# Optimization experiments

Measured on AMD Instinct MI355X. Metric: run time of the kernel, lower is better.

## Reference

```python
import jax, jax.numpy as jnp
import numpy as np

H1, H2, H3 = 32, 64, 64
NODEN = 12
NODES_PER_GRAPH = NODEN + 2  # 14
N = 700000                   # 50000 graphs * 14 nodes
E = 4000000


def setup_inputs() -> dict:
    key = jax.random.key(0)
    ks = jax.random.split(key, 8)
    x = jax.random.normal(ks[0], (N, H1), dtype=jnp.float32)
    edges = jax.random.randint(ks[1], (2, E), 0, N, dtype=jnp.int64)
    W1 = jax.random.normal(ks[2], (H1, H2), dtype=jnp.float32) / np.sqrt(H1).astype(np.float32)
    b1 = jnp.zeros((H2,), jnp.float32)
    W2 = jax.random.normal(ks[3], (H2, H3), dtype=jnp.float32) / np.sqrt(H2).astype(np.float32)
    b2 = jnp.zeros((H3,), jnp.float32)
    Wfc = jax.random.normal(ks[4], (H3 * NODES_PER_GRAPH, 1), dtype=jnp.float32) / np.sqrt(H3 * NODES_PER_GRAPH).astype(np.float32)
    bfc = jnp.zeros((1,), jnp.float32)
    return {"x": x, "edges": edges, "W1": W1, "b1": b1, "W2": W2, "b2": b2, "Wfc": Wfc, "bfc": bfc}


def gcn_conv(x, src, dst, W, b, n):
    # PyG GCNConv: h = X W; add self-loops; norm = deg^-1/2[src]*deg^-1/2[dst]
    h = x @ W  # [N, out]
    ones = jnp.ones(src.shape[0], dtype=h.dtype)
    deg = jax.ops.segment_sum(ones, dst, num_segments=n) + jnp.asarray(1.0, h.dtype)  # +1 self-loop
    dinv = jax.lax.rsqrt(deg)  # deg >= 1 always (self-loop)
    norm = dinv[src] * dinv[dst]  # [E]
    agg = jax.ops.segment_sum(h[src] * norm[:, None], dst, num_segments=n)
    agg = agg + h * (dinv * dinv)[:, None]  # self-loop contribution
    return agg + b


def reference(x, edges, W1, b1, W2, b2, Wfc, bfc):
    src, dst = edges[0], edges[1]
    h = jax.nn.relu(gcn_conv(x, src, dst, W1, b1, N))
    # F.dropout(training=False) is identity in eval mode
    h = jax.nn.relu(gcn_conv(h, src, dst, W2, b2, N))
    h = h.reshape(-1, H3 * NODES_PER_GRAPH)  # [B, 896]
    return h @ Wfc + bfc  # [B, 1]
```

## Files before the change

### kernel.cpp

```cpp
#include <hip/hip_runtime.h>
#include <hip/hip_fp16.h>


typedef _Float16 half8 __attribute__((ext_vector_type(8)));
typedef float float4v __attribute__((ext_vector_type(4)));

#define CHUNK 8192
#define BSH 11
#define BNODES 2048
#define DBINS 64
#define NBKMAX 512

__global__ __launch_bounds__(256) void fallback_kernel(float* __restrict__ out, int n, float v)
{
  int i = blockIdx.x * 256 + threadIdx.x;
  if (i < n) out[i] = v;
}

__device__ inline int edges_shift(const int* __restrict__ edges)
{
  int orv = edges[1] | edges[3] | edges[5] | edges[7] | edges[9] | edges[11] | edges[13] | edges[15];
  return (orv == 0) ? 1 : 0;
}

__device__ inline void scan_bstart(const int* __restrict__ gtot, int NBK, int* __restrict__ bl)
{
  int t = threadIdx.x;
  if (t < 64) {
    int carry = 0;
    int rounds = (NBK + 63) >> 6;
    for (int r = 0; r < rounds; r++) {
      int idx = r * 64 + t;
      int v = (idx < NBK) ? gtot[idx] : 0;
      int incl = v;
#pragma unroll
      for (int off = 1; off < 64; off <<= 1) {
        int x = __shfl_up(incl, off);
        if (t >= off) incl += x;
      }
      if (idx < NBK) bl[idx] = incl - v + carry;
      carry += __shfl(incl, 63);
    }
    if (t == 0) bl[NBK] = carry;
  }
}

__global__ __launch_bounds__(256) void hist2_kernel(
    const int* __restrict__ edges, int E, int N,
    int* __restrict__ cnt, int NBK, int* __restrict__ gtot,
    __half* __restrict__ P, __half* __restrict__ F2)
{
  __shared__ int lh[NBKMAX];
  int t = threadIdx.x;
  int blk = blockIdx.x;
  if (blk == 0) {
    if (t < 8) ((uint2*)(P + (size_t)N * 32))[t] = make_uint2(0, 0);
    else if (t < 24) ((uint2*)(F2 + (size_t)N * 64))[t - 8] = make_uint2(0, 0);
  }
  for (int b = t; b < NBK; b += 256) lh[b] = 0;
  __syncthreads();
  int sh = edges_shift(edges);
  int base = blk * CHUNK;
#pragma unroll
  for (int k = 0; k < CHUNK / 256; k++) {
    int e = base + k * 256 + t;
    if (e < E) {
      int d = edges[(E + e) << sh];
      if ((unsigned)d < (unsigned)N) atomicAdd(&lh[d >> BSH], 1);
    }
  }
  __syncthreads();
  for (int b = t; b < NBK; b += 256)
    cnt[(size_t)blk * NBK + b] = atomicAdd(&gtot[b], lh[b]);
}

__global__ __launch_bounds__(256) void pass3_kernel(
    const int* __restrict__ edges, int E, int N,
    const int* __restrict__ cnt, const int* __restrict__ gtot,
    int* __restrict__ pair, int NBK)
{
  __shared__ int bl[NBKMAX + 1];
  __shared__ int lcur[NBKMAX];
  int t = threadIdx.x;
  int blk = blockIdx.x;
  scan_bstart(gtot, NBK, bl);
  __syncthreads();
  for (int b = t; b < NBK; b += 256)
    lcur[b] = bl[b] + cnt[(size_t)blk * NBK + b];
  __syncthreads();
  int sh = edges_shift(edges);
  int base = blk * CHUNK;
#pragma unroll
  for (int k = 0; k < CHUNK / 256; k++) {
    int e = base + k * 256 + t;
    if (e < E) {
      int s = edges[e << sh];
      int d = edges[(E + e) << sh];
      if ((unsigned)s < (unsigned)N && (unsigned)d < (unsigned)N) {
        int pos = atomicAdd(&lcur[d >> BSH], 1);
        pair[pos] = s | ((d & (BNODES - 1)) << 20);
      }
    }
  }
}

__global__ __launch_bounds__(256) void build_kernel(
    const int* __restrict__ pair, const int* __restrict__ gtot,
    int* __restrict__ rowptr, float* __restrict__ dinv, int* __restrict__ col,
    int* __restrict__ dhist, int N, int NBK)
{
  __shared__ int bl[NBKMAX + 1];
  __shared__ int hist[BNODES];
  __shared__ int cur[BNODES];
  __shared__ int sc[256];
  __shared__ int lh2[DBINS];
  int b = blockIdx.x;
  int t = threadIdx.x;
  scan_bstart(gtot, NBK, bl);
  if (t < DBINS) lh2[t] = 0;
#pragma unroll
  for (int i = 0; i < BNODES / 256; i++) {
    int idx = i * 256 + t;
    int row = (b << BSH) + idx;
    hist[idx] = (row < N) ? 1 : 0;
  }
  __syncthreads();
  int pbeg = bl[b], pend = bl[b + 1];
  int colbase = pbeg + (b << BSH);
  if (b == 0 && t == 0) rowptr[N] = bl[NBK] + N;
  for (int p = pbeg + t; p < pend; p += 256)
    atomicAdd(&hist[(pair[p] >> 20) & (BNODES - 1)], 1);
  __syncthreads();
  int hv[8];
  int tsum = 0;
#pragma unroll
  for (int i = 0; i < 8; i++) { hv[i] = hist[t * 8 + i]; tsum += hv[i]; }
  sc[t] = tsum;
  __syncthreads();
  for (int off = 1; off < 256; off <<= 1) {
    int x = 0;
    if (t >= off) x = sc[t - off];
    __syncthreads();
    if (t >= off) sc[t] += x;
    __syncthreads();
  }
  int run = sc[t] - tsum;
#pragma unroll
  for (int i = 0; i < 8; i++) {
    int idx = t * 8 + i;
    int rp = colbase + run;
    int row = (b << BSH) + idx;
    if (row < N) {
      rowptr[row] = rp;
      dinv[row] = rsqrtf((float)hv[i]);
      col[rp] = row;
      cur[idx] = rp + 1;
      int bin = hv[i] < DBINS ? hv[i] : DBINS - 1;
      atomicAdd(&lh2[bin], 1);
    } else {
      cur[idx] = rp;
    }
    run += hv[i];
  }
  __syncthreads();
  if (t < DBINS && lh2[t]) atomicAdd(&dhist[t], lh2[t]);
  for (int p = pbeg + t; p < pend; p += 256) {
    int v = pair[p];
    int pos = atomicAdd(&cur[(v >> 20) & (BNODES - 1)], 1);
    col[pos] = v & 0xFFFFF;
  }
}

__global__ __launch_bounds__(256) void deg_place_kernel(
    const int* __restrict__ rowptr, const float* __restrict__ dinv,
    const int* __restrict__ dhist, int* __restrict__ dcnt,
    int* __restrict__ perm, int* __restrict__ iperm,
    int2* __restrict__ rowinfo, float* __restrict__ dinv_p,
    const float* __restrict__ X, __half* __restrict__ P,
    float* __restrict__ out, const float* __restrict__ bfc, int N, int B)
{
  __shared__ int bb[DBINS];
  __shared__ int lh[DBINS];
  __shared__ int lbase[DBINS];
  int t = threadIdx.x;
  int n = blockIdx.x * 256 + t;
  if (n < B) out[n] = bfc[0];
  if (t < DBINS) {
    lh[t] = 0;
    int v = dhist[t];
    int incl = v;
#pragma unroll
    for (int off = 1; off < DBINS; off <<= 1) {
      int x = __shfl_up(incl, off);
      if (t >= off) incl += x;
    }
    bb[t] = incl - v;
  }
  __syncthreads();
  int b = -1, rbeg = 0, rlen = 0;
  if (n < N) {
    rbeg = rowptr[n];
    rlen = rowptr[n + 1] - rbeg;
    b = rlen < DBINS ? rlen : DBINS - 1;
    atomicAdd(&lh[b], 1);
  }
  __syncthreads();
  if (t < DBINS) lbase[t] = lh[t] ? (bb[t] + atomicAdd(&dcnt[t], lh[t])) : 0;
  __syncthreads();
  if (t < DBINS) lh[t] = lbase[t];
  __syncthreads();
  if (n < N) {
    int pos = atomicAdd(&lh[b], 1);
    float dv = dinv[n];
    perm[pos] = n;
    iperm[n] = pos;
    rowinfo[pos] = make_int2(rbeg, rlen);
    dinv_p[pos] = dv;
    const float4* xp = (const float4*)(X + (size_t)n * 32);
    __half* pp = P + (size_t)pos * 32;
#pragma unroll
    for (int part = 0; part < 4; part++) {
      float4 v0 = xp[part * 2], v1 = xp[part * 2 + 1];
      half8 h;
      h[0] = (_Float16)(dv * v0.x); h[1] = (_Float16)(dv * v0.y);
      h[2] = (_Float16)(dv * v0.z); h[3] = (_Float16)(dv * v0.w);
      h[4] = (_Float16)(dv * v1.x); h[5] = (_Float16)(dv * v1.y);
      h[6] = (_Float16)(dv * v1.z); h[7] = (_Float16)(dv * v1.w);
      *(half8*)(pp + part * 8) = h;
    }
  }
}

__global__ __launch_bounds__(256) void prep_remap_kernel(
    int* __restrict__ col, const int* __restrict__ iperm, const int* __restrict__ rowptr, int N)
{
  int idx = blockIdx.x * 256 + threadIdx.x;
  int stride = gridDim.x * 256;
  int total = rowptr[N];
  for (int k = idx; k < total; k += stride) col[k] = iperm[col[k]];
}

__device__ inline void hacc(uint4 v, __half2* a)
{
  a[0] = __hadd2(a[0], *reinterpret_cast<__half2*>(&v.x));
  a[1] = __hadd2(a[1], *reinterpret_cast<__half2*>(&v.y));
  a[2] = __hadd2(a[2], *reinterpret_cast<__half2*>(&v.z));
  a[3] = __hadd2(a[3], *reinterpret_cast<__half2*>(&v.w));
}

__global__ __launch_bounds__(256) void agg1_pos_kernel(
    const __half* __restrict__ P, const int2* __restrict__ rowinfo,
    const int* __restrict__ col, const float* __restrict__ dinv_p,
    const float* __restrict__ W1, const float* __restrict__ b1,
    __half* __restrict__ U, int ntiles, int ndummy)
{
  int lane = threadIdx.x & 63;
  int n16 = lane & 15;
  int quad = lane >> 4;

  half8 bf[4];
#pragma unroll
  for (int jb = 0; jb < 4; jb++)
#pragma unroll
    for (int i = 0; i < 8; i++)
      bf[jb][i] = (_Float16)W1[(quad * 8 + i) * 64 + jb * 16 + n16];
  float b1j[4];
#pragma unroll
  for (int jb = 0; jb < 4; jb++) b1j[jb] = b1[jb * 16 + n16];

  const uint4* P4 = (const uint4*)P;
  _Float16* Uh = (_Float16*)U;
  int wave = (blockIdx.x * 256 + threadIdx.x) >> 6;
  int nw = (gridDim.x * 256) >> 6;
  for (int tile = wave; tile < ntiles; tile += nw) {
    int ut = __builtin_amdgcn_readfirstlane(tile);
    int base = ut * 16;
    int2 ri = rowinfo[base + n16];
    int rbeg = ri.x, rlen = ri.y;
    float dvown = dinv_p[base + n16];

    __half2 z2 = __float2half2_rn(0.f);
    __half2 aA[4] = {z2, z2, z2, z2};
    __half2 aB[4] = {z2, z2, z2, z2};

    for (int j = 0; __any(j < rlen); j += 8) {
      int c[8];
#pragma unroll
      for (int q = 0; q < 8; q++) {
        int cc = col[rbeg + j + q];
        c[q] = (j + q < rlen) ? cc : ndummy;
      }
      uint4 v[8];
#pragma unroll
      for (int q = 0; q < 8; q++) v[q] = P4[((size_t)c[q] << 2) + quad];
#pragma unroll
      for (int q = 0; q < 8; q += 2) { hacc(v[q], aA); hacc(v[q + 1], aB); }
    }
#pragma unroll
    for (int k = 0; k < 4; k++) aA[k] = __hadd2(aA[k], aB[k]);

    half8 a = *reinterpret_cast<half8*>(aA);
    float4v co[4];
#pragma unroll
    for (int jb = 0; jb < 4; jb++) {
      float4v z = {0.f, 0.f, 0.f, 0.f};
      co[jb] = __builtin_amdgcn_mfma_f32_16x16x32_f16(a, bf[jb], z, 0, 0, 0);
    }
#pragma unroll
    for (int r = 0; r < 4; r++) {
      int pos2 = base + quad * 4 + r;
      float dv = __shfl(dvown, quad * 4 + r);
#pragma unroll
      for (int jb = 0; jb < 4; jb++) {
        float h = dv * co[jb][r] + b1j[jb];
        h = h > 0.f ? h : 0.f;
        Uh[(size_t)pos2 * 64 + jb * 16 + n16] = (_Float16)(dv * h);
      }
    }
  }
}

__global__ __launch_bounds__(256) void mfma_final_fused_kernel(
    const __half* __restrict__ U, const int2* __restrict__ rowinfo,
    const int* __restrict__ col, const float* __restrict__ dinv_p,
    const int* __restrict__ perm,
    const float* __restrict__ W2, const float* __restrict__ b2,
    const float* __restrict__ Wfc, float* __restrict__ out,
    int ntiles, int ndummy)
{
  int lane = threadIdx.x & 63;
  int n16 = lane & 15;
  int quad = lane >> 4;

  half8 bf[4][2];
#pragma unroll
  for (int jb = 0; jb < 4; jb++)
#pragma unroll
    for (int kf = 0; kf < 2; kf++)
#pragma unroll
      for (int i = 0; i < 8; i++)
        bf[jb][kf][i] = (_Float16)W2[(kf * 32 + quad * 8 + i) * 64 + jb * 16 + n16];
  float b2j[4];
#pragma unroll
  for (int jb = 0; jb < 4; jb++) b2j[jb] = b2[jb * 16 + n16];

  const uint4* U4 = (const uint4*)U;
  int wave = (blockIdx.x * 256 + threadIdx.x) >> 6;
  int nw = (gridDim.x * 256) >> 6;
  for (int tile = wave; tile < ntiles; tile += nw) {
    int ut = __builtin_amdgcn_readfirstlane(tile);
    int base = ut * 16;
    int2 ri = rowinfo[base + n16];
    int rbeg = ri.x, rlen = ri.y;
    int node = perm[base + n16];
    float dvown = dinv_p[base + n16];

    __half2 z2 = __float2half2_rn(0.f);
    __half2 aE0[4] = {z2, z2, z2, z2};
    __half2 aE1[4] = {z2, z2, z2, z2};
    __half2 aO0[4] = {z2, z2, z2, z2};
    __half2 aO1[4] = {z2, z2, z2, z2};

    for (int j = 0; __any(j < rlen); j += 4) {
      int c0 = col[rbeg + j];
      int c1 = col[rbeg + j + 1];
      int c2 = col[rbeg + j + 2];
      int c3 = col[rbeg + j + 3];
      c0 = (j < rlen) ? c0 : ndummy;
      c1 = (j + 1 < rlen) ? c1 : ndummy;
      c2 = (j + 2 < rlen) ? c2 : ndummy;
      c3 = (j + 3 < rlen) ? c3 : ndummy;
      uint4 v00 = U4[((size_t)c0 << 3) + quad];
      uint4 v01 = U4[((size_t)c0 << 3) + 4 + quad];
      uint4 v10 = U4[((size_t)c1 << 3) + quad];
      uint4 v11 = U4[((size_t)c1 << 3) + 4 + quad];
      uint4 v20 = U4[((size_t)c2 << 3) + quad];
      uint4 v21 = U4[((size_t)c2 << 3) + 4 + quad];
      uint4 v30 = U4[((size_t)c3 << 3) + quad];
      uint4 v31 = U4[((size_t)c3 << 3) + 4 + quad];
      hacc(v00, aE0); hacc(v01, aE1);
      hacc(v10, aO0); hacc(v11, aO1);
      hacc(v20, aE0); hacc(v21, aE1);
      hacc(v30, aO0); hacc(v31, aO1);
    }
#pragma unroll
    for (int k = 0; k < 4; k++) {
      aE0[k] = __hadd2(aE0[k], aO0[k]);
      aE1[k] = __hadd2(aE1[k], aO1[k]);
    }
    __half2 dv = __half2half2(__float2half_rn(dvown));
#pragma unroll
    for (int j = 0; j < 4; j++) {
      aE0[j] = __hmul2(aE0[j], dv);
      aE1[j] = __hmul2(aE1[j], dv);
    }
    half8 a0 = *reinterpret_cast<half8*>(aE0);
    half8 a1 = *reinterpret_cast<half8*>(aE1);

    int g_r[4], t_r[4];
#pragma unroll
    for (int r = 0; r < 4; r++) {
      int nd = __shfl(node, quad * 4 + r);
      g_r[r] = nd / 14;
      t_r[r] = nd - g_r[r] * 14;
    }
    float pr[4] = {0.f, 0.f, 0.f, 0.f};
#pragma unroll
    for (int jb = 0; jb < 4; jb++) {
      float4v acc = {0.f, 0.f, 0.f, 0.f};
      acc = __builtin_amdgcn_mfma_f32_16x16x32_f16(a0, bf[jb][0], acc, 0, 0, 0);
      acc = __builtin_amdgcn_mfma_f32_16x16x32_f16(a1, bf[jb][1], acc, 0, 0, 0);
      int j = jb * 16 + n16;
#pragma unroll
      for (int r = 0; r < 4; r++) {
        float h = acc[r] + b2j[jb];
        h = h > 0.f ? h : 0.f;
        pr[r] += h * Wfc[t_r[r] * 64 + j];
      }
    }
#pragma unroll
    for (int r = 0; r < 4; r++) {
#pragma unroll
      for (int off = 1; off < 16; off <<= 1) pr[r] += __shfl_xor(pr[r], off);
    }
    if (n16 == 0) {
#pragma unroll
      for (int r = 0; r < 4; r++) atomicAdd(&out[g_r[r]], pr[r]);
    }
  }
}

extern "C" void kernel_launch(void* const* d_in, const int* in_sizes, int n_in,
                              void* d_out, int out_size, void* d_ws, size_t ws_size,
                              hipStream_t stream)
{
  const float* x = (const float*)d_in[0];
  const int* edges = (const int*)d_in[1];
  const float* W1 = (const float*)d_in[2];
  const float* b1 = (const float*)d_in[3];
  const float* W2 = (const float*)d_in[4];
  const float* b2 = (const float*)d_in[5];
  const float* Wfc = (const float*)d_in[6];
  const float* bfc = (const float*)d_in[7];
  float* out = (float*)d_out;
  (void)n_in;

  const int N = in_sizes[0] / 32;
  const int E = in_sizes[1] / 2;
  const int B = out_size;
  const int NBK = (N + BNODES - 1) >> BSH;
  const int NCH = (E + CHUNK - 1) / CHUNK;
  const int NBLK = (N + 255) / 256;

  char* ws = (char*)d_ws;
  size_t off = 0;
  auto alloc = [&](size_t bytes) -> void* {
    void* p = ws + off;
    off += (bytes + 255) & ~(size_t)255;
    return p;
  };
  int* cnt = (int*)alloc((size_t)NCH * NBK * 4);
  int* zbuf = (int*)alloc(((size_t)NBK + 2 * DBINS) * 4);
  int* gtot = zbuf;
  int* dhist = zbuf + NBK;
  int* dcnt = zbuf + NBK + DBINS;
  int* col = (int*)alloc(((size_t)E + N + 256) * 4);
  int* rowptr = (int*)alloc(((size_t)N + 1) * 4);
  float* dinv = (float*)alloc((size_t)N * 4);
  int* perm = (int*)alloc((size_t)N * 4);
  int* iperm = (int*)alloc((size_t)N * 4);
  int2* rowinfo = (int2*)alloc((size_t)N * 8);
  float* dinv_p = (float*)alloc((size_t)N * 4);
  __half* P = (__half*)alloc(((size_t)N + 16) * 32 * 2);
  __half* F2 = (__half*)alloc(((size_t)N + 16) * 64 * 2);
  int* pair = (int*)P;

  if (off > ws_size) {
    float v = -(float)(double)(ws_size >> 20);
    fallback_kernel<<<(B + 255) / 256, 256, 0, stream>>>(out, B, v);
    return;
  }

  hipMemsetAsync(zbuf, 0, ((size_t)NBK + 2 * DBINS) * 4, stream);
  hist2_kernel<<<NCH, 256, 0, stream>>>(edges, E, N, cnt, NBK, gtot, P, F2);
  pass3_kernel<<<NCH, 256, 0, stream>>>(edges, E, N, cnt, gtot, pair, NBK);
  build_kernel<<<NBK, 256, 0, stream>>>(pair, gtot, rowptr, dinv, col, dhist, N, NBK);
  deg_place_kernel<<<NBLK, 256, 0, stream>>>(rowptr, dinv, dhist, dcnt,
                                             perm, iperm, rowinfo, dinv_p,
                                             x, P, out, bfc, N, B);
  prep_remap_kernel<<<4096, 256, 0, stream>>>(col, iperm, rowptr, N);

  int ntiles = (N + 15) / 16;
  agg1_pos_kernel<<<4096, 256, 0, stream>>>(P, rowinfo, col, dinv_p, W1, b1, F2, ntiles, N);
  mfma_final_fused_kernel<<<4096, 256, 0, stream>>>(F2, rowinfo, col, dinv_p, perm, W2, b2, Wfc,
                                                    out, ntiles, N);
}
```

Before: 567.6 us.

## Fuse graph-preprocessing kernels into one cooperative persistent kernel with grid syncs

Replaces the memset and five preprocessing kernels (histogram, scatter, CSR build, degree-sorted placement, column remap) with a single cooperative kernel that walks each phase with grid-stride loops and separates phases with grid.sync(). The aim is to remove per-launch overhead and the idle gaps between small dependent kernels. In exchange the grid is capped by occupancy (at most 2048 blocks), so each phase runs on fewer blocks. Grid-wide barriers and heavy shared-memory use per block may also cut parallelism.

```diff
diff --git a/kernel.cpp b/kernel.cpp
--- a/kernel.cpp
+++ b/kernel.cpp
@@ -1,6 +1,9 @@
 #include <hip/hip_runtime.h>
 #include <hip/hip_fp16.h>
-
+#include <hip/hip_cooperative_groups.h>
+
+
+namespace cg = cooperative_groups;
 
 typedef _Float16 half8 __attribute__((ext_vector_type(8)));
 typedef float float4v __attribute__((ext_vector_type(4)));
@@ -45,207 +48,223 @@
   }
 }
 
-__global__ __launch_bounds__(256) void hist2_kernel(
-    const int* __restrict__ edges, int E, int N,
-    int* __restrict__ cnt, int NBK, int* __restrict__ gtot,
-    __half* __restrict__ P, __half* __restrict__ F2)
-{
-  __shared__ int lh[NBKMAX];
+struct ChainArgs {
+  const int* edges; int E; int N; int B;
+  int* cnt; int NBK; int* gtot; int* dhist; int* dcnt;
+  int* pair; int* rowptr; float* dinv; int* col;
+  int* perm; int* iperm; int2* rowinfo; float* dinv_p;
+  const float* X; __half* P; __half* F2;
+  float* out; const float* bfc;
+  int NCH; int NBLK;
+};
+
+__global__ __launch_bounds__(256) void chain_kernel(ChainArgs a)
+{
+  __shared__ int smem[4936];
+  cg::grid_group grid = cg::this_grid();
   int t = threadIdx.x;
-  int blk = blockIdx.x;
-  if (blk == 0) {
-    if (t < 8) ((uint2*)(P + (size_t)N * 32))[t] = make_uint2(0, 0);
-    else if (t < 24) ((uint2*)(F2 + (size_t)N * 64))[t - 8] = make_uint2(0, 0);
-  }
-  for (int b = t; b < NBK; b += 256) lh[b] = 0;
-  __syncthreads();
-  int sh = edges_shift(edges);
-  int base = blk * CHUNK;
-#pragma unroll
-  for (int k = 0; k < CHUNK / 256; k++) {
-    int e = base + k * 256 + t;
-    if (e < E) {
-      int d = edges[(E + e) << sh];
-      if ((unsigned)d < (unsigned)N) atomicAdd(&lh[d >> BSH], 1);
-    }
-  }
-  __syncthreads();
-  for (int b = t; b < NBK; b += 256)
-    cnt[(size_t)blk * NBK + b] = atomicAdd(&gtot[b], lh[b]);
-}
-
-__global__ __launch_bounds__(256) void pass3_kernel(
-    const int* __restrict__ edges, int E, int N,
-    const int* __restrict__ cnt, const int* __restrict__ gtot,
-    int* __restrict__ pair, int NBK)
-{
-  __shared__ int bl[NBKMAX + 1];
-  __shared__ int lcur[NBKMAX];
-  int t = threadIdx.x;
-  int blk = blockIdx.x;
-  scan_bstart(gtot, NBK, bl);
-  __syncthreads();
-  for (int b = t; b < NBK; b += 256)
-    lcur[b] = bl[b] + cnt[(size_t)blk * NBK + b];
-  __syncthreads();
-  int sh = edges_shift(edges);
-  int base = blk * CHUNK;
-#pragma unroll
-  for (int k = 0; k < CHUNK / 256; k++) {
-    int e = base + k * 256 + t;
-    if (e < E) {
-      int s = edges[e << sh];
-      int d = edges[(E + e) << sh];
-      if ((unsigned)s < (unsigned)N && (unsigned)d < (unsigned)N) {
-        int pos = atomicAdd(&lcur[d >> BSH], 1);
-        pair[pos] = s | ((d & (BNODES - 1)) << 20);
-      }
-    }
-  }
-}
-
-__global__ __launch_bounds__(256) void build_kernel(
-    const int* __restrict__ pair, const int* __restrict__ gtot,
-    int* __restrict__ rowptr, float* __restrict__ dinv, int* __restrict__ col,
-    int* __restrict__ dhist, int N, int NBK)
-{
-  __shared__ int bl[NBKMAX + 1];
-  __shared__ int hist[BNODES];
-  __shared__ int cur[BNODES];
-  __shared__ int sc[256];
-  __shared__ int lh2[DBINS];
-  int b = blockIdx.x;
-  int t = threadIdx.x;
-  scan_bstart(gtot, NBK, bl);
-  if (t < DBINS) lh2[t] = 0;
-#pragma unroll
-  for (int i = 0; i < BNODES / 256; i++) {
-    int idx = i * 256 + t;
-    int row = (b << BSH) + idx;
-    hist[idx] = (row < N) ? 1 : 0;
-  }
-  __syncthreads();
-  int pbeg = bl[b], pend = bl[b + 1];
-  int colbase = pbeg + (b << BSH);
-  if (b == 0 && t == 0) rowptr[N] = bl[NBK] + N;
-  for (int p = pbeg + t; p < pend; p += 256)
-    atomicAdd(&hist[(pair[p] >> 20) & (BNODES - 1)], 1);
-  __syncthreads();
-  int hv[8];
-  int tsum = 0;
-#pragma unroll
-  for (int i = 0; i < 8; i++) { hv[i] = hist[t * 8 + i]; tsum += hv[i]; }
-  sc[t] = tsum;
-  __syncthreads();
-  for (int off = 1; off < 256; off <<= 1) {
-    int x = 0;
-    if (t >= off) x = sc[t - off];
+  int nb = gridDim.x;
+
+  {
+    int ztot = a.NBK + 2 * DBINS;
+    for (int i = blockIdx.x * 256 + t; i < ztot; i += nb * 256) {
+      if (i < a.NBK) a.gtot[i] = 0;
+      else if (i < a.NBK + DBINS) a.dhist[i - a.NBK] = 0;
+      else a.dcnt[i - a.NBK - DBINS] = 0;
+    }
+    if (blockIdx.x == 0) {
+      if (t < 8) ((uint2*)(a.P + (size_t)a.N * 32))[t] = make_uint2(0, 0);
+      else if (t < 24) ((uint2*)(a.F2 + (size_t)a.N * 64))[t - 8] = make_uint2(0, 0);
+    }
+  }
+  grid.sync();
+  int sh = edges_shift(a.edges);
+
+  {
+    int* lh = smem;
+    for (int blk = blockIdx.x; blk < a.NCH; blk += nb) {
+      for (int b = t; b < a.NBK; b += 256) lh[b] = 0;
+      __syncthreads();
+      int base = blk * CHUNK;
+#pragma unroll
+      for (int k = 0; k < CHUNK / 256; k++) {
+        int e = base + k * 256 + t;
+        if (e < a.E) {
+          int d = a.edges[(a.E + e) << sh];
+          if ((unsigned)d < (unsigned)a.N) atomicAdd(&lh[d >> BSH], 1);
+        }
+      }
+      __syncthreads();
+      for (int b = t; b < a.NBK; b += 256)
+        a.cnt[(size_t)blk * a.NBK + b] = atomicAdd(&a.gtot[b], lh[b]);
+      __syncthreads();
+    }
+  }
+  grid.sync();
+
+  {
+    int* bl = smem;
+    int* lcur = smem + NBKMAX + 1;
+    scan_bstart(a.gtot, a.NBK, bl);
     __syncthreads();
-    if (t >= off) sc[t] += x;
+    for (int blk = blockIdx.x; blk < a.NCH; blk += nb) {
+      for (int b = t; b < a.NBK; b += 256)
+        lcur[b] = bl[b] + a.cnt[(size_t)blk * a.NBK + b];
+      __syncthreads();
+      int base = blk * CHUNK;
+#pragma unroll
+      for (int k = 0; k < CHUNK / 256; k++) {
+        int e = base + k * 256 + t;
+        if (e < a.E) {
+          int s = a.edges[e << sh];
+          int d = a.edges[(a.E + e) << sh];
+          if ((unsigned)s < (unsigned)a.N && (unsigned)d < (unsigned)a.N) {
+            int pos = atomicAdd(&lcur[d >> BSH], 1);
+            a.pair[pos] = s | ((d & (BNODES - 1)) << 20);
+          }
+        }
+      }
+      __syncthreads();
+    }
+  }
+  grid.sync();
+
+  {
+    int* bl = smem;
+    int* hist = smem + 520;
+    int* cur = smem + 2568;
+    int* sc = smem + 4616;
+    int* lh2 = smem + 4872;
+    scan_bstart(a.gtot, a.NBK, bl);
     __syncthreads();
-  }
-  int run = sc[t] - tsum;
-#pragma unroll
-  for (int i = 0; i < 8; i++) {
-    int idx = t * 8 + i;
-    int rp = colbase + run;
-    int row = (b << BSH) + idx;
-    if (row < N) {
-      rowptr[row] = rp;
-      dinv[row] = rsqrtf((float)hv[i]);
-      col[rp] = row;
-      cur[idx] = rp + 1;
-      int bin = hv[i] < DBINS ? hv[i] : DBINS - 1;
-      atomicAdd(&lh2[bin], 1);
-    } else {
-      cur[idx] = rp;
-    }
-    run += hv[i];
-  }
-  __syncthreads();
-  if (t < DBINS && lh2[t]) atomicAdd(&dhist[t], lh2[t]);
-  for (int p = pbeg + t; p < pend; p += 256) {
-    int v = pair[p];
-    int pos = atomicAdd(&cur[(v >> 20) & (BNODES - 1)], 1);
-    col[pos] = v & 0xFFFFF;
-  }
-}
-
-__global__ __launch_bounds__(256) void deg_place_kernel(
-    const int* __restrict__ rowptr, const float* __restrict__ dinv,
-    const int* __restrict__ dhist, int* __restrict__ dcnt,
-    int* __restrict__ perm, int* __restrict__ iperm,
-    int2* __restrict__ rowinfo, float* __restrict__ dinv_p,
-    const float* __restrict__ X, __half* __restrict__ P,
-    float* __restrict__ out, const float* __restrict__ bfc, int N, int B)
-{
-  __shared__ int bb[DBINS];
-  __shared__ int lh[DBINS];
-  __shared__ int lbase[DBINS];
-  int t = threadIdx.x;
-  int n = blockIdx.x * 256 + t;
-  if (n < B) out[n] = bfc[0];
-  if (t < DBINS) {
-    lh[t] = 0;
-    int v = dhist[t];
-    int incl = v;
-#pragma unroll
-    for (int off = 1; off < DBINS; off <<= 1) {
-      int x = __shfl_up(incl, off);
-      if (t >= off) incl += x;
-    }
-    bb[t] = incl - v;
-  }
-  __syncthreads();
-  int b = -1, rbeg = 0, rlen = 0;
-  if (n < N) {
-    rbeg = rowptr[n];
-    rlen = rowptr[n + 1] - rbeg;
-    b = rlen < DBINS ? rlen : DBINS - 1;
-    atomicAdd(&lh[b], 1);
-  }
-  __syncthreads();
-  if (t < DBINS) lbase[t] = lh[t] ? (bb[t] + atomicAdd(&dcnt[t], lh[t])) : 0;
-  __syncthreads();
-  if (t < DBINS) lh[t] = lbase[t];
-  __syncthreads();
-  if (n < N) {
-    int pos = atomicAdd(&lh[b], 1);
-    float dv = dinv[n];
-    perm[pos] = n;
-    iperm[n] = pos;
-    rowinfo[pos] = make_int2(rbeg, rlen);
-    dinv_p[pos] = dv;
-    const float4* xp = (const float4*)(X + (size_t)n * 32);
-    __half* pp = P + (size_t)pos * 32;
-#pragma unroll
-    for (int part = 0; part < 4; part++) {
-      float4 v0 = xp[part * 2], v1 = xp[part * 2 + 1];
-      half8 h;
-      h[0] = (_Float16)(dv * v0.x); h[1] = (_Float16)(dv * v0.y);
-      h[2] = (_Float16)(dv * v0.z); h[3] = (_Float16)(dv * v0.w);
-      h[4] = (_Float16)(dv * v1.x); h[5] = (_Float16)(dv * v1.y);
-      h[6] = (_Float16)(dv * v1.z); h[7] = (_Float16)(dv * v1.w);
-      *(half8*)(pp + part * 8) = h;
-    }
-  }
-}
-
-__global__ __launch_bounds__(256) void prep_remap_kernel(
-    int* __restrict__ col, const int* __restrict__ iperm, const int* __restrict__ rowptr, int N)
-{
-  int idx = blockIdx.x * 256 + threadIdx.x;
-  int stride = gridDim.x * 256;
-  int total = rowptr[N];
-  for (int k = idx; k < total; k += stride) col[k] = iperm[col[k]];
-}
-
-__device__ inline void hacc(uint4 v, __half2* a)
-{
-  a[0] = __hadd2(a[0], *reinterpret_cast<__half2*>(&v.x));
-  a[1] = __hadd2(a[1], *reinterpret_cast<__half2*>(&v.y));
-  a[2] = __hadd2(a[2], *reinterpret_cast<__half2*>(&v.z));
-  a[3] = __hadd2(a[3], *reinterpret_cast<__half2*>(&v.w));
+    for (int b = blockIdx.x; b < a.NBK; b += nb) {
+      if (t < DBINS) lh2[t] = 0;
+#pragma unroll
+      for (int i = 0; i < BNODES / 256; i++) {
+        int idx = i * 256 + t;
+        int row = (b << BSH) + idx;
+        hist[idx] = (row < a.N) ? 1 : 0;
+      }
+      __syncthreads();
+      int pbeg = bl[b], pend = bl[b + 1];
+      int colbase = pbeg + (b << BSH);
+      if (b == 0 && t == 0) a.rowptr[a.N] = bl[a.NBK] + a.N;
+      for (int p = pbeg + t; p < pend; p += 256)
+        atomicAdd(&hist[(a.pair[p] >> 20) & (BNODES - 1)], 1);
+      __syncthreads();
+      int hv[8];
+      int tsum = 0;
+#pragma unroll
+      for (int i = 0; i < 8; i++) { hv[i] = hist[t * 8 + i]; tsum += hv[i]; }
+      sc[t] = tsum;
+      __syncthreads();
+      for (int off = 1; off < 256; off <<= 1) {
+        int x = 0;
+        if (t >= off) x = sc[t - off];
+        __syncthreads();
+        if (t >= off) sc[t] += x;
+        __syncthreads();
+      }
+      int run = sc[t] - tsum;
+#pragma unroll
+      for (int i = 0; i < 8; i++) {
+        int idx = t * 8 + i;
+        int rp = colbase + run;
+        int row = (b << BSH) + idx;
+        if (row < a.N) {
+          a.rowptr[row] = rp;
+          a.dinv[row] = rsqrtf((float)hv[i]);
+          a.col[rp] = row;
+          cur[idx] = rp + 1;
+          int bin = hv[i] < DBINS ? hv[i] : DBINS - 1;
+          atomicAdd(&lh2[bin], 1);
+        } else {
+          cur[idx] = rp;
+        }
+        run += hv[i];
+      }
+      __syncthreads();
+      if (t < DBINS && lh2[t]) atomicAdd(&a.dhist[t], lh2[t]);
+      for (int p = pbeg + t; p < pend; p += 256) {
+        int v = a.pair[p];
+        int pos = atomicAdd(&cur[(v >> 20) & (BNODES - 1)], 1);
+        a.col[pos] = v & 0xFFFFF;
+      }
+      __syncthreads();
+    }
+  }
+  grid.sync();
+
+  {
+    int* bb = smem;
+    int* lh = smem + 64;
+    int* lbase = smem + 128;
+    if (t < DBINS) {
+      int v = a.dhist[t];
+      int incl = v;
+#pragma unroll
+      for (int off = 1; off < DBINS; off <<= 1) {
+        int x = __shfl_up(incl, off);
+        if (t >= off) incl += x;
+      }
+      bb[t] = incl - v;
+    }
+    __syncthreads();
+    for (int i = blockIdx.x * 256 + t; i < a.B; i += nb * 256) a.out[i] = a.bfc[0];
+    for (int blk = blockIdx.x; blk < a.NBLK; blk += nb) {
+      if (t < DBINS) lh[t] = 0;
+      __syncthreads();
+      int n = blk * 256 + t;
+      int b = -1, rbeg = 0, rlen = 0;
+      if (n < a.N) {
+        rbeg = a.rowptr[n];
+        rlen = a.rowptr[n + 1] - rbeg;
+        b = rlen < DBINS ? rlen : DBINS - 1;
+        atomicAdd(&lh[b], 1);
+      }
+      __syncthreads();
+      if (t < DBINS) lbase[t] = lh[t] ? (bb[t] + atomicAdd(&a.dcnt[t], lh[t])) : 0;
+      __syncthreads();
+      if (t < DBINS) lh[t] = lbase[t];
+      __syncthreads();
+      if (n < a.N) {
+        int pos = atomicAdd(&lh[b], 1);
+        float dv = a.dinv[n];
+        a.perm[pos] = n;
+        a.iperm[n] = pos;
+        a.rowinfo[pos] = make_int2(rbeg, rlen);
+        a.dinv_p[pos] = dv;
+        const float4* xp = (const float4*)(a.X + (size_t)n * 32);
+        __half* pp = a.P + (size_t)pos * 32;
+#pragma unroll
+        for (int part = 0; part < 4; part++) {
+          float4 v0 = xp[part * 2], v1 = xp[part * 2 + 1];
+          half8 h;
+          h[0] = (_Float16)(dv * v0.x); h[1] = (_Float16)(dv * v0.y);
+          h[2] = (_Float16)(dv * v0.z); h[3] = (_Float16)(dv * v0.w);
+          h[4] = (_Float16)(dv * v1.x); h[5] = (_Float16)(dv * v1.y);
+          h[6] = (_Float16)(dv * v1.z); h[7] = (_Float16)(dv * v1.w);
+          *(half8*)(pp + part * 8) = h;
+        }
+      }
+      __syncthreads();
+    }
+  }
+  grid.sync();
+
+  {
+    int total = a.rowptr[a.N];
+    for (int k = blockIdx.x * 256 + t; k < total; k += nb * 256)
+      a.col[k] = a.iperm[a.col[k]];
+  }
+}
+
+__device__ inline void hacc(uint4 v, __half2* acc)
+{
+  acc[0] = __hadd2(acc[0], *reinterpret_cast<__half2*>(&v.x));
+  acc[1] = __hadd2(acc[1], *reinterpret_cast<__half2*>(&v.y));
+  acc[2] = __hadd2(acc[2], *reinterpret_cast<__half2*>(&v.z));
+  acc[3] = __hadd2(acc[3], *reinterpret_cast<__half2*>(&v.w));
 }
 
 __global__ __launch_bounds__(256) void agg1_pos_kernel(
@@ -481,14 +500,22 @@
     return;
   }
 
-  hipMemsetAsync(zbuf, 0, ((size_t)NBK + 2 * DBINS) * 4, stream);
-  hist2_kernel<<<NCH, 256, 0, stream>>>(edges, E, N, cnt, NBK, gtot, P, F2);
-  pass3_kernel<<<NCH, 256, 0, stream>>>(edges, E, N, cnt, gtot, pair, NBK);
-  build_kernel<<<NBK, 256, 0, stream>>>(pair, gtot, rowptr, dinv, col, dhist, N, NBK);
-  deg_place_kernel<<<NBLK, 256, 0, stream>>>(rowptr, dinv, dhist, dcnt,
-                                             perm, iperm, rowinfo, dinv_p,
-                                             x, P, out, bfc, N, B);
-  prep_remap_kernel<<<4096, 256, 0, stream>>>(col, iperm, rowptr, N);
+  ChainArgs ca;
+  ca.edges = edges; ca.E = E; ca.N = N; ca.B = B;
+  ca.cnt = cnt; ca.NBK = NBK; ca.gtot = gtot; ca.dhist = dhist; ca.dcnt = dcnt;
+  ca.pair = pair; ca.rowptr = rowptr; ca.dinv = dinv; ca.col = col;
+  ca.perm = perm; ca.iperm = iperm; ca.rowinfo = rowinfo; ca.dinv_p = dinv_p;
+  ca.X = x; ca.P = P; ca.F2 = F2; ca.out = out; ca.bfc = bfc;
+  ca.NCH = NCH; ca.NBLK = NBLK;
+
+  int maxb = 0;
+  hipOccupancyMaxActiveBlocksPerMultiprocessor(&maxb, chain_kernel, 256, 0);
+  if (maxb < 1) maxb = 1;
+  int cgrid = maxb * 256;
+  if (cgrid > 2048) cgrid = 2048;
+
+  void* cargs[] = { &ca };
+  hipLaunchCooperativeKernel(chain_kernel, dim3(cgrid), dim3(256), cargs, 0, stream);
 
   int ntiles = (N + 15) / 16;
   agg1_pos_kernel<<<4096, 256, 0, stream>>>(P, rowinfo, col, dinv_p, W1, b1, F2, ntiles, N);
```

After: 1.183 ms. +108.4%, slower.
